# Kernel optimization log

Measured on AMD Instinct MI355X. Metric: run time of the kernel, lower is better.

## Reference

```python
import jax, jax.numpy as jnp
import numpy as np

NUM_EMB = 512
EMB_DIM = 64

def conv1d(x, w, b=None, stride=1, padding=0):
    # x: (N,C,L), w: (O,I,K) torch Conv1d layout
    out = jax.lax.conv_general_dilated(x, w, (stride,), [(padding, padding)],
                                       dimension_numbers=('NCH', 'OIH', 'NCH'))
    if b is not None:
        out = out + b[None, :, None]
    return out

def conv_transpose1d(x, w, b, stride, padding):
    # w: (I,O,K) torch ConvTranspose1d layout -> flip kernel, swap I/O
    k = w.shape[2]
    wf = jnp.flip(w, 2).transpose(1, 0, 2)  # (O,I,K)
    pad = k - 1 - padding
    out = jax.lax.conv_general_dilated(x, wf, (1,), [(pad, pad)],
                                       lhs_dilation=(stride,),
                                       dimension_numbers=('NCH', 'OIH', 'NCH'))
    return out + b[None, :, None]

def residual_block(x, w1, w2):
    # ReLU -> conv3(pad1, no bias) -> ReLU -> conv1(no bias), residual add
    h = conv1d(jax.nn.relu(x), w1, None, 1, 1)
    h = conv1d(jax.nn.relu(h), w2, None, 1, 0)
    return x + h

def residual_stack(x, r0_w1, r0_w2, r1_w1, r1_w2):
    x = residual_block(x, r0_w1, r0_w2)
    x = residual_block(x, r1_w1, r1_w2)
    return jax.nn.relu(x)

def vq(z, emb):
    # z: (B, C=64, T); torch VectorQuantizerEMA eval path (decay=0, not training)
    B, C, T = z.shape
    inputs = z.transpose(0, 2, 1)                 # (B,T,C)
    flat = inputs.reshape(-1, C)                  # (B*T, C)
    d = (jnp.sum(flat * flat, axis=1, keepdims=True)
         + jnp.sum(emb * emb, axis=1)
         - 2.0 * flat @ emb.T)                    # (B*T, K)
    idx = jnp.argmin(d, axis=1)
    enc = jax.nn.one_hot(idx, NUM_EMB, dtype=flat.dtype)  # (B*T, K)
    q = (enc @ emb).reshape(B, T, C)
    # straight-through estimator
    q = inputs + jax.lax.stop_gradient(q - inputs)
    return q.transpose(0, 2, 1)                   # (B,C,T)

def reference(x, enc_w1, enc_b1, enc_w2, enc_b2, enc_w3, enc_b3,
              enc_r0_w1, enc_r0_w2, enc_r1_w1, enc_r1_w2,
              prevq_w, prevq_b, emb,
              dec_w1, dec_b1, dec_r0_w1, dec_r0_w2, dec_r1_w1, dec_r1_w2,
              dect1_w, dect1_b, dect2_w, dect2_b):
    # Encoder
    h = jax.nn.relu(conv1d(x, enc_w1, enc_b1, 2, 1))
    h = jax.nn.relu(conv1d(h, enc_w2, enc_b2, 2, 1))
    h = conv1d(h, enc_w3, enc_b3, 1, 1)
    h = residual_stack(h, enc_r0_w1, enc_r0_w2, enc_r1_w1, enc_r1_w2)
    # pre-VQ 1x1 conv
    z = conv1d(h, prevq_w, prevq_b, 1, 0)
    # Vector quantization
    q = vq(z, emb)
    # Decoder
    d = conv1d(q, dec_w1, dec_b1, 1, 1)
    d = residual_stack(d, dec_r0_w1, dec_r0_w2, dec_r1_w1, dec_r1_w2)
    d = jax.nn.relu(conv_transpose1d(d, dect1_w, dect1_b, 2, 1))
    return conv_transpose1d(d, dect2_w, dect2_b, 2, 1)

def setup_inputs() -> dict:
    key = jax.random.key(0)
    ks = jax.random.split(key, 25)
    def n(k, shape, s=0.05):
        return jax.random.normal(k, shape, dtype=jnp.float32) * s
    return {
        'x': jax.random.normal(ks[0], (16, 768, 4096), dtype=jnp.float32),
        'enc_w1': n(ks[1], (32, 768, 4)), 'enc_b1': n(ks[2], (32,)),
        'enc_w2': n(ks[3], (64, 32, 4)), 'enc_b2': n(ks[4], (64,)),
        'enc_w3': n(ks[5], (64, 64, 3)), 'enc_b3': n(ks[6], (64,)),
        'enc_r0_w1': n(ks[7], (32, 64, 3)), 'enc_r0_w2': n(ks[8], (64, 32, 1)),
        'enc_r1_w1': n(ks[9], (32, 64, 3)), 'enc_r1_w2': n(ks[10], (64, 32, 1)),
        'prevq_w': n(ks[11], (64, 64, 1)), 'prevq_b': n(ks[12], (64,)),
        'emb': jax.random.normal(ks[13], (512, 64), dtype=jnp.float32),
        'dec_w1': n(ks[14], (64, 64, 3)), 'dec_b1': n(ks[15], (64,)),
        'dec_r0_w1': n(ks[16], (32, 64, 3)), 'dec_r0_w2': n(ks[17], (64, 32, 1)),
        'dec_r1_w1': n(ks[18], (32, 64, 3)), 'dec_r1_w2': n(ks[19], (64, 32, 1)),
        'dect1_w': n(ks[20], (64, 32, 4)), 'dect1_b': n(ks[21], (32,)),
        'dect2_w': n(ks[22], (32, 64, 4)), 'dect2_b': n(ks[23], (64,)),
    }
```

## Files before the change

### kernel.cpp

```cpp
#include <hip/hip_runtime.h>


typedef _Float16 half8 __attribute__((ext_vector_type(8)));
typedef float f32x4 __attribute__((ext_vector_type(4)));
union H8u { half8 h; int4 i; };
union P4u { _Float16 e[4]; int2 u; };

__device__ __forceinline__ void splitf(float v, _Float16& h, _Float16& l) {
  h = (_Float16)v; l = (_Float16)((v - (float)h) * 2048.0f);
}
#define INV2048 (1.0f / 2048.0f)

#define OFF_C1   0
#define OFF_C2   98304
#define OFF_C3   106496
#define OFF_ER0A 122880
#define OFF_ER0B 131072
#define OFF_ER1A 133120
#define OFF_ER1B 141312
#define OFF_PQ   143360
#define OFF_DW1  147456
#define OFF_DR0A 163840
#define OFF_DR0B 172032
#define OFF_DR1A 174080
#define OFF_DR1B 182272
#define OFF_T1   184320
#define OFF_T2   200704
#define WTOT     217088

struct WPtrs {
  const float *c1, *c2, *c3, *er0a, *er0b, *er1a, *er1b, *pq,
              *dw1, *dr0a, *dr0b, *dr1a, *dr1b, *t1, *t2;
};

__device__ __forceinline__ int tpose_kt(int par, int tap) {
  if (par == 0) { if (tap == 0) return 3; if (tap == 1) return 1; }
  else          { if (tap == 1) return 2; if (tap == 2) return 0; }
  return -1;
}

__global__ __launch_bounds__(256) void prep_k(WPtrs P, _Float16* __restrict__ WH,
                                              _Float16* __restrict__ WL) {
  int s = blockIdx.x * 256 + threadIdx.x;
  if (s >= WTOT) return;
  float v = 0.f;
  if (s < OFF_C2) {
    int t = s, kkblk = t >> 11, rem = t & 2047, col = rem >> 6, kkin = rem & 63;
    int kk = kkblk * 64 + kkin;
    v = P.c1[col * 3072 + kk];
  } else if (s < OFF_C3) {
    int t = s - OFF_C2, co = t >> 7, kk = t & 127;
    v = P.c2[(co * 32 + (kk >> 2)) * 4 + (kk & 3)];
  } else if (s < OFF_ER0A) {
    int t = s - OFF_C3, co = t >> 8, kk = t & 255, tap = kk & 3;
    if (tap < 3) v = P.c3[(co * 64 + (kk >> 2)) * 3 + tap];
  } else if (s < OFF_ER0B) {
    int t = s - OFF_ER0A, co = t >> 8, kk = t & 255, tap = kk & 3;
    if (tap < 3) v = P.er0a[(co * 64 + (kk >> 2)) * 3 + tap];
  } else if (s < OFF_ER1A) {
    int t = s - OFF_ER0B; v = P.er0b[t];
  } else if (s < OFF_ER1B) {
    int t = s - OFF_ER1A, co = t >> 8, kk = t & 255, tap = kk & 3;
    if (tap < 3) v = P.er1a[(co * 64 + (kk >> 2)) * 3 + tap];
  } else if (s < OFF_PQ) {
    int t = s - OFF_ER1B; v = P.er1b[t];
  } else if (s < OFF_DW1) {
    int t = s - OFF_PQ; v = P.pq[t];
  } else if (s < OFF_DR0A) {
    int t = s - OFF_DW1, co = t >> 8, kk = t & 255, tap = kk & 3;
    if (tap < 3) v = P.dw1[(co * 64 + (kk >> 2)) * 3 + tap];
  } else if (s < OFF_DR0B) {
    int t = s - OFF_DR0A, co = t >> 8, kk = t & 255, tap = kk & 3;
    if (tap < 3) v = P.dr0a[(co * 64 + (kk >> 2)) * 3 + tap];
  } else if (s < OFF_DR1A) {
    int t = s - OFF_DR0B; v = P.dr0b[t];
  } else if (s < OFF_DR1B) {
    int t = s - OFF_DR1A, co = t >> 8, kk = t & 255, tap = kk & 3;
    if (tap < 3) v = P.dr1a[(co * 64 + (kk >> 2)) * 3 + tap];
  } else if (s < OFF_T1) {
    int t = s - OFF_DR1B; v = P.dr1b[t];
  } else if (s < OFF_T2) {
    int t = s - OFF_T1, nn = t >> 8, kk = t & 255;
    int par = nn >> 5, co = nn & 31, ci = kk >> 2;
    int kt = tpose_kt(par, kk & 3);
    if (kt >= 0) v = P.t1[(ci * 32 + co) * 4 + kt];
  } else {
    int t = s - OFF_T2, nn = t >> 7, kk = t & 127;
    int par = nn >> 6, co = nn & 63, ci = kk >> 2;
    int kt = tpose_kt(par, kk & 3);
    if (kt >= 0) v = P.t2[(ci * 64 + co) * 4 + kt];
  }
  _Float16 h, l; splitf(v, h, l);
  WH[s] = h; WL[s] = l;
}

__global__ __launch_bounds__(256, 4) void conv1_k(
    const float* __restrict__ x, const _Float16* __restrict__ WH,
    const _Float16* __restrict__ WL, float* __restrict__ Pout, int cpp) {
  __shared__ _Float16 Hs[2][16 * 136];
  __shared__ _Float16 Ls[2][16 * 136];
  __shared__ _Float16 Bhs[2][32 * 64];
  __shared__ _Float16 Bls[2][32 * 64];
  const int tid = threadIdx.x;
  const int w = tid >> 6, lane = tid & 63, lm = lane & 15, quad = lane >> 4;
  const int m0 = blockIdx.x * 64, n = blockIdx.y, kpart = blockIdx.z;
  const int r = w * 16 + lm;
  const int pb = 2 * m0 - 1;
  const float* xn = x + (size_t)n * 768 * 4096;
  const int r0s = tid / 33, c0s = tid % 33;
  const int r1s = (256 + tid) / 33, c1s = (256 + tid) % 33;
  const int r2s = (512 + tid) / 33, c2s = (512 + tid) % 33;
  const int bcol = tid >> 3, bslot = tid & 7;
  const int bdst = bcol * 64 + ((bslot ^ (bcol & 7)) << 3);

  f32x4 acc1[2], acc2[2];
#pragma unroll
  for (int j = 0; j < 2; ++j)
#pragma unroll
    for (int rr = 0; rr < 4; ++rr) { acc1[j][rr] = 0.f; acc2[j][rr] = 0.f; }

  const int cb0 = kpart * cpp;
  float4 sv0, sv1, sv2;
  H8u bhv, blv;

#define C1_LD1(SV, RS, CS) { \
    int p0 = pb + 4 * (CS); \
    const float* rp = xn + (size_t)(chb + (RS)) * 4096; \
    if (p0 >= 0 && p0 + 3 < 4096) SV = *(const float4*)(rp + p0); \
    else { \
      SV.x = (p0   >= 0 && p0   < 4096) ? rp[p0]   : 0.f; \
      SV.y = (p0+1 >= 0 && p0+1 < 4096) ? rp[p0+1] : 0.f; \
      SV.z = (p0+2 >= 0 && p0+2 < 4096) ? rp[p0+2] : 0.f; \
      SV.w = (p0+3 >= 0 && p0+3 < 4096) ? rp[p0+3] : 0.f; } }

#define C1_LOAD(cc) { \
    int chb = (cb0 + (cc)) * 16; \
    C1_LD1(sv0, r0s, c0s) \
    C1_LD1(sv1, r1s, c1s) \
    if (tid < 16) C1_LD1(sv2, r2s, c2s) \
    bhv.i = *(const int4*)(WH + (size_t)(cb0 + (cc)) * 2048 + tid * 8); \
    blv.i = *(const int4*)(WL + (size_t)(cb0 + (cc)) * 2048 + tid * 8); }

#define C1_WR1(SV, RS, CS, B) { \
    P4u ph, pl; \
    splitf(SV.x, ph.e[0], pl.e[0]); splitf(SV.y, ph.e[1], pl.e[1]); \
    splitf(SV.z, ph.e[2], pl.e[2]); splitf(SV.w, ph.e[3], pl.e[3]); \
    *(int2*)(&Hs[B][(RS) * 136 + 4 * (CS)]) = ph.u; \
    *(int2*)(&Ls[B][(RS) * 136 + 4 * (CS)]) = pl.u; }

#define C1_WRITE(B) { \
    C1_WR1(sv0, r0s, c0s, B) \
    C1_WR1(sv1, r1s, c1s, B) \
    if (tid < 16) C1_WR1(sv2, r2s, c2s, B) \
    *(int4*)(&Bhs[B][bdst]) = bhv.i; \
    *(int4*)(&Bls[B][bdst]) = blv.i; }

#define C1_COMP(B) { \
    const uint* Hdw = (const uint*)(&Hs[B][0]); \
    const uint* Ldw = (const uint*)(&Ls[B][0]); \
    _Pragma("unroll") \
    for (int ks = 0; ks < 2; ++ks) { \
      const int ci0 = ks * 8 + quad * 2; \
      const int bse = ci0 * 68 + r; \
      H8u ah, al; \
      ah.i.x = Hdw[bse];      ah.i.y = Hdw[bse + 1]; \
      ah.i.z = Hdw[bse + 68]; ah.i.w = Hdw[bse + 69]; \
      al.i.x = Ldw[bse];      al.i.y = Ldw[bse + 1]; \
      al.i.z = Ldw[bse + 68]; al.i.w = Ldw[bse + 69]; \
      const int sA = ((4 * ks + quad) ^ (lm & 7)) << 3; \
      H8u b0h, b0l, b1h, b1l; \
      b0h.i = *(const int4*)(&Bhs[B][lm * 64 + sA]); \
      b0l.i = *(const int4*)(&Bls[B][lm * 64 + sA]); \
      b1h.i = *(const int4*)(&Bhs[B][(16 + lm) * 64 + sA]); \
      b1l.i = *(const int4*)(&Bls[B][(16 + lm) * 64 + sA]); \
      acc1[0] = __builtin_amdgcn_mfma_f32_16x16x32_f16(ah.h, b0h.h, acc1[0], 0,0,0); \
      acc2[0] = __builtin_amdgcn_mfma_f32_16x16x32_f16(ah.h, b0l.h, acc2[0], 0,0,0); \
      acc2[0] = __builtin_amdgcn_mfma_f32_16x16x32_f16(al.h, b0h.h, acc2[0], 0,0,0); \
      acc1[1] = __builtin_amdgcn_mfma_f32_16x16x32_f16(ah.h, b1h.h, acc1[1], 0,0,0); \
      acc2[1] = __builtin_amdgcn_mfma_f32_16x16x32_f16(ah.h, b1l.h, acc2[1], 0,0,0); \
      acc2[1] = __builtin_amdgcn_mfma_f32_16x16x32_f16(al.h, b1h.h, acc2[1], 0,0,0); \
    } }

  C1_LOAD(0);
  C1_WRITE(0);
  __syncthreads();
#pragma unroll 1
  for (int cc = 0; cc < cpp; ++cc) {
    const int cur = cc & 1;
    if (cc + 1 < cpp) C1_LOAD(cc + 1);
    C1_COMP(cur);
    if (cc + 1 < cpp) C1_WRITE(cur ^ 1);
    __syncthreads();
  }

#pragma unroll
  for (int j = 0; j < 2; ++j) {
    int col = j * 16 + lm;
    float4 o;
    o.x = acc1[j][0] + acc2[j][0] * INV2048;
    o.y = acc1[j][1] + acc2[j][1] * INV2048;
    o.z = acc1[j][2] + acc2[j][2] * INV2048;
    o.w = acc1[j][3] + acc2[j][3] * INV2048;
    *(float4*)(Pout + (size_t)kpart * (16 * 32 * 2048)
               + ((size_t)n * 32 + col) * 2048 + m0 + w * 16 + quad * 4) = o;
  }
#undef C1_LD1
#undef C1_LOAD
#undef C1_WR1
#undef C1_WRITE
#undef C1_COMP
}

template<int CI, int KP, int NT, int STRIDE,
         bool RELU_IN, bool RELU_OUT, bool BIAS, bool TPOSE, bool RESBLK,
         bool PSUM = false>
__global__ __launch_bounds__(256) void gconv(
    const float* __restrict__ in, const _Float16* __restrict__ WH,
    const _Float16* __restrict__ WL, const float* __restrict__ bias,
    const _Float16* __restrict__ W2H, const _Float16* __restrict__ W2L,
    float* __restrict__ out, int Lin, int Lout,
    const float* __restrict__ inbias, int nparts, int pplane) {
  constexpr int CP = 32 * STRIDE + 4;
  constexpr int CP4 = CP / 4;
  constexpr int AP = KP + 8;
  constexpr int KS = KP / 32;
  constexpr int NTW = (NT == 2) ? 1 : NT / 2;
  __shared__ float xs[CI * CP];
  __shared__ _Float16 Ah[32 * AP];
  __shared__ _Float16 Al[32 * AP];
  __shared__ _Float16 A2h[RESBLK ? 32 * 40 : 1];
  __shared__ _Float16 A2l[RESBLK ? 32 * 40 : 1];
  const int tid = threadIdx.x;
  const int w = tid >> 6, lane = tid & 63, lm = lane & 15, quad = lane >> 4;
  const int mt = w >> 1, ntb = (w & 1) * NTW;
  const int m0 = blockIdx.x * 32, n = blockIdx.y;
  const int base = m0 * STRIDE - 1;
  const float* inN = in + (size_t)n * CI * Lin;
  constexpr int SLOTS = CI * CP4;
#pragma unroll
  for (int it = 0; it < (SLOTS + 255) / 256; ++it) {
    int idx = it * 256 + tid;
    if (idx < SLOTS) {
      int row = idx / CP4, c4 = idx % CP4;
      int p0 = base + c4 * 4;
      const float* rp = inN + (size_t)row * Lin;
      float4 v;
      if (PSUM) {
        v.x = 0.f; v.y = 0.f; v.z = 0.f; v.w = 0.f;
        bool i0 = (p0   >= 0 && p0   < Lin);
        bool i1 = (p0+1 >= 0 && p0+1 < Lin);
        bool i2 = (p0+2 >= 0 && p0+2 < Lin);
        bool i3 = (p0+3 >= 0 && p0+3 < Lin);
        bool full = (p0 >= 0 && p0 + 3 < Lin);
        for (int p = 0; p < nparts; ++p) {
          const float* rpp = rp + (size_t)p * pplane;
          if (full) {
            float4 t = *(const float4*)(rpp + p0);
            v.x += t.x; v.y += t.y; v.z += t.z; v.w += t.w;
          } else {
            if (i0) v.x += rpp[p0];
            if (i1) v.y += rpp[p0+1];
            if (i2) v.z += rpp[p0+2];
            if (i3) v.w += rpp[p0+3];
          }
        }
        float bv = inbias[row];
        v.x = i0 ? fmaxf(v.x + bv, 0.f) : 0.f;
        v.y = i1 ? fmaxf(v.y + bv, 0.f) : 0.f;
        v.z = i2 ? fmaxf(v.z + bv, 0.f) : 0.f;
        v.w = i3 ? fmaxf(v.w + bv, 0.f) : 0.f;
      } else {
        if (p0 >= 0 && p0 + 3 < Lin) v = *(const float4*)(rp + p0);
        else {
          v.x = (p0   >= 0 && p0   < Lin) ? rp[p0]   : 0.f;
          v.y = (p0+1 >= 0 && p0+1 < Lin) ? rp[p0+1] : 0.f;
          v.z = (p0+2 >= 0 && p0+2 < Lin) ? rp[p0+2] : 0.f;
          v.w = (p0+3 >= 0 && p0+3 < Lin) ? rp[p0+3] : 0.f;
        }
      }
      *(float4*)(&xs[row * CP + c4 * 4]) = v;
    }
  }
  __syncthreads();
#pragma unroll
  for (int it = 0; it < (32 * CI) / 256; ++it) {
    int slot = it * 256 + tid;
    int ci = slot & (CI - 1), m = slot / CI;
    const float* xr = &xs[ci * CP + STRIDE * m];
    float a0 = xr[0], a1 = xr[1], a2 = xr[2], a3 = xr[3];
    if (RELU_IN) { a0 = fmaxf(a0,0.f); a1 = fmaxf(a1,0.f);
                   a2 = fmaxf(a2,0.f); a3 = fmaxf(a3,0.f); }
    P4u ph, pl;
    splitf(a0, ph.e[0], pl.e[0]); splitf(a1, ph.e[1], pl.e[1]);
    splitf(a2, ph.e[2], pl.e[2]); splitf(a3, ph.e[3], pl.e[3]);
    *(int2*)(&Ah[m * AP + ci * 4]) = ph.u;
    *(int2*)(&Al[m * AP + ci * 4]) = pl.u;
  }
  __syncthreads();
  f32x4 acc1[NTW], acc2[NTW];
#pragma unroll
  for (int j = 0; j < NTW; ++j)
#pragma unroll
    for (int r = 0; r < 4; ++r) { acc1[j][r] = 0.f; acc2[j][r] = 0.f; }
  H8u bh[2][NTW], bl[2][NTW];
#pragma unroll
  for (int j = 0; j < NTW; ++j) {
    int col = (ntb + j) * 16 + lm;
    bh[0][j].i = *(const int4*)(WH + (size_t)col * KP + quad * 8);
    bl[0][j].i = *(const int4*)(WL + (size_t)col * KP + quad * 8);
  }
#pragma unroll
  for (int ks = 0; ks < KS; ++ks) {
    int cur = ks & 1;
    if (ks + 1 < KS) {
#pragma unroll
      for (int j = 0; j < NTW; ++j) {
        int col = (ntb + j) * 16 + lm;
        bh[cur ^ 1][j].i = *(const int4*)(WH + (size_t)col * KP + (ks+1) * 32 + quad * 8);
        bl[cur ^ 1][j].i = *(const int4*)(WL + (size_t)col * KP + (ks+1) * 32 + quad * 8);
      }
    }
    H8u ah, al;
    ah.i = *(const int4*)(&Ah[(mt * 16 + lm) * AP + ks * 32 + quad * 8]);
    al.i = *(const int4*)(&Al[(mt * 16 + lm) * AP + ks * 32 + quad * 8]);
#pragma unroll
    for (int j = 0; j < NTW; ++j) {
      acc1[j] = __builtin_amdgcn_mfma_f32_16x16x32_f16(ah.h, bh[cur][j].h, acc1[j], 0,0,0);
      acc2[j] = __builtin_amdgcn_mfma_f32_16x16x32_f16(ah.h, bl[cur][j].h, acc2[j], 0,0,0);
      acc2[j] = __builtin_amdgcn_mfma_f32_16x16x32_f16(al.h, bh[cur][j].h, acc2[j], 0,0,0);
    }
  }
  if (RESBLK) {
    int co2 = (w & 1) * 16 + lm;
#pragma unroll
    for (int r = 0; r < 4; ++r) {
      float hv = fmaxf(acc1[0][r] + acc2[0][r] * INV2048, 0.f);
      _Float16 hh, hl; splitf(hv, hh, hl);
      int m = mt * 16 + quad * 4 + r;
      A2h[m * 40 + co2] = hh; A2l[m * 40 + co2] = hl;
    }
    __syncthreads();
    f32x4 c1[2], c2[2];
#pragma unroll
    for (int j = 0; j < 2; ++j)
#pragma unroll
      for (int r = 0; r < 4; ++r) { c1[j][r] = 0.f; c2[j][r] = 0.f; }
    H8u a2h, a2l;
    a2h.i = *(const int4*)(&A2h[(mt * 16 + lm) * 40 + quad * 8]);
    a2l.i = *(const int4*)(&A2l[(mt * 16 + lm) * 40 + quad * 8]);
    int ntb2 = (w & 1) * 2;
#pragma unroll
    for (int j = 0; j < 2; ++j) {
      int col = (ntb2 + j) * 16 + lm;
      H8u wbh, wbl;
      wbh.i = *(const int4*)(W2H + col * 32 + quad * 8);
      wbl.i = *(const int4*)(W2L + col * 32 + quad * 8);
      c1[j] = __builtin_amdgcn_mfma_f32_16x16x32_f16(a2h.h, wbh.h, c1[j], 0,0,0);
      c2[j] = __builtin_amdgcn_mfma_f32_16x16x32_f16(a2h.h, wbl.h, c2[j], 0,0,0);
      c2[j] = __builtin_amdgcn_mfma_f32_16x16x32_f16(a2l.h, wbh.h, c2[j], 0,0,0);
    }
#pragma unroll
    for (int j = 0; j < 2; ++j) {
      int col = (ntb2 + j) * 16 + lm;
      float4 o;
#pragma unroll
      for (int r = 0; r < 4; ++r) {
        int m = mt * 16 + quad * 4 + r;
        float res = xs[col * CP + m + 1];
        ((float*)&o)[r] = res + c1[j][r] + c2[j][r] * INV2048;
      }
      *(float4*)(out + ((size_t)n * 64 + col) * Lout + m0 + mt * 16 + quad * 4) = o;
    }
  } else {
    constexpr int CO = TPOSE ? NT * 8 : NT * 16;
#pragma unroll
    for (int j = 0; j < NTW; ++j) {
      int col = (ntb + j) * 16 + lm;
      int par = TPOSE ? (col / CO) : 0;
      int co  = TPOSE ? (col % CO) : col;
      float bv = BIAS ? bias[co] : 0.f;
      float vr[4];
#pragma unroll
      for (int r = 0; r < 4; ++r) {
        float v = acc1[j][r] + acc2[j][r] * INV2048 + bv;
        vr[r] = RELU_OUT ? fmaxf(v, 0.f) : v;
      }
      if (TPOSE) {
#pragma unroll
        for (int r = 0; r < 4; ++r) {
          int m = m0 + mt * 16 + quad * 4 + r;
          out[((size_t)n * CO + co) * Lout + 2 * m + par] = vr[r];
        }
      } else {
        float4 o; o.x = vr[0]; o.y = vr[1]; o.z = vr[2]; o.w = vr[3];
        *(float4*)(out + ((size_t)n * CO + co) * Lout + m0 + mt * 16 + quad * 4) = o;
      }
    }
  }
}

__global__ void enorm_k(const float* __restrict__ emb, float* __restrict__ en) {
  int e = blockIdx.x * blockDim.x + threadIdx.x;
  if (e >= 512) return;
  float s = 0.f;
  const float* r = emb + (size_t)e * 64;
  for (int c = 0; c < 64; ++c) s = fmaf(r[c], r[c], s);
  en[e] = s;
}

__global__ __launch_bounds__(256) void vq_fused(
    const float* __restrict__ sIn, const _Float16* __restrict__ PQH,
    const _Float16* __restrict__ PQL, const float* __restrict__ pqb,
    const float* __restrict__ emb, const float* __restrict__ en,
    float* __restrict__ q) {
  __shared__ float xs[64 * 68];
  __shared__ _Float16 Ah[64 * 72];
  __shared__ _Float16 Al[64 * 72];
  __shared__ float zl[64 * 65];
  __shared__ float dred[4 * 64];
  __shared__ int   ired[4 * 64];
  __shared__ int   idxs[64];
  const int tid = threadIdx.x;
  const int w = tid >> 6, lane = tid & 63, lm = lane & 15, quad = lane >> 4;
  const int n = blockIdx.y, t0 = blockIdx.x * 64;
#pragma unroll
  for (int it = 0; it < 4; ++it) {
    int idx = it * 256 + tid;
    int row = idx >> 4, c4 = idx & 15;
    float4 v = *(const float4*)(sIn + ((size_t)n * 64 + row) * 1024 + t0 + c4 * 4);
    *(float4*)(&xs[row * 68 + c4 * 4]) = v;
  }
  __syncthreads();
#pragma unroll
  for (int it = 0; it < 16; ++it) {
    int slot = it * 256 + tid;
    int ci = slot & 63, t = slot >> 6;
    float v = fmaxf(xs[ci * 68 + t], 0.f);
    _Float16 h, l; splitf(v, h, l);
    Ah[t * 72 + ci] = h; Al[t * 72 + ci] = l;
  }
  __syncthreads();
  f32x4 a1[4], a2[4];
#pragma unroll
  for (int j = 0; j < 4; ++j)
#pragma unroll
    for (int r = 0; r < 4; ++r) { a1[j][r] = 0.f; a2[j][r] = 0.f; }
#pragma unroll
  for (int ks = 0; ks < 2; ++ks) {
    H8u ah, al;
    ah.i = *(const int4*)(&Ah[(w * 16 + lm) * 72 + ks * 32 + quad * 8]);
    al.i = *(const int4*)(&Al[(w * 16 + lm) * 72 + ks * 32 + quad * 8]);
#pragma unroll
    for (int j = 0; j < 4; ++j) {
      int col = j * 16 + lm;
      H8u bh, bl;
      bh.i = *(const int4*)(PQH + col * 64 + ks * 32 + quad * 8);
      bl.i = *(const int4*)(PQL + col * 64 + ks * 32 + quad * 8);
      a1[j] = __builtin_amdgcn_mfma_f32_16x16x32_f16(ah.h, bh.h, a1[j], 0,0,0);
      a2[j] = __builtin_amdgcn_mfma_f32_16x16x32_f16(ah.h, bl.h, a2[j], 0,0,0);
      a2[j] = __builtin_amdgcn_mfma_f32_16x16x32_f16(al.h, bh.h, a2[j], 0,0,0);
    }
  }
#pragma unroll
  for (int j = 0; j < 4; ++j) {
    int col = j * 16 + lm;
    float bv = pqb[col];
#pragma unroll
    for (int r = 0; r < 4; ++r) {
      int t = w * 16 + quad * 4 + r;
      zl[t * 65 + col] = a1[j][r] + a2[j][r] * INV2048 + bv;
    }
  }
  __syncthreads();
  int tt = tid & 63, cq = tid >> 6;
  float zv[64];
#pragma unroll
  for (int c = 0; c < 64; ++c) zv[c] = zl[tt * 65 + c];
  float best = 1e30f; int bidx = 0;
  for (int e = cq * 128; e < cq * 128 + 128; ++e) {
    const float* er = emb + (size_t)e * 64;
    float dot = 0.f;
#pragma unroll
    for (int c = 0; c < 64; ++c) dot = fmaf(zv[c], er[c], dot);
    float d = en[e] - 2.f * dot;
    if (d < best) { best = d; bidx = e; }
  }
  dred[cq * 64 + tt] = best;
  ired[cq * 64 + tt] = bidx;
  __syncthreads();
  if (cq == 0) {
    for (int j = 1; j < 4; ++j) {
      float d = dred[j * 64 + tt]; int i2 = ired[j * 64 + tt];
      if (d < best || (d == best && i2 < bidx)) { best = d; bidx = i2; }
    }
    idxs[tt] = bidx;
  }
  __syncthreads();
  for (int it = 0; it < 16; ++it) {
    int c = cq * 16 + it;
    q[((size_t)n * 64 + c) * 1024 + t0 + tt] = emb[(size_t)idxs[tt] * 64 + c];
  }
}

extern "C" void kernel_launch(void* const* d_in, const int* in_sizes, int n_in,
                              void* d_out, int out_size, void* d_ws, size_t ws_size,
                              hipStream_t stream) {
  const float* x        = (const float*)d_in[0];
  const float* enc_b1   = (const float*)d_in[2];
  const float* enc_b2   = (const float*)d_in[4];
  const float* enc_b3   = (const float*)d_in[6];
  const float* prevq_b  = (const float*)d_in[12];
  const float* emb      = (const float*)d_in[13];
  const float* dec_b1   = (const float*)d_in[15];
  const float* dect1_b  = (const float*)d_in[21];
  const float* dect2_b  = (const float*)d_in[23];
  float* out = (float*)d_out;

  WPtrs P;
  P.c1  = (const float*)d_in[1];  P.c2  = (const float*)d_in[3];
  P.c3  = (const float*)d_in[5];  P.er0a = (const float*)d_in[7];
  P.er0b = (const float*)d_in[8]; P.er1a = (const float*)d_in[9];
  P.er1b = (const float*)d_in[10]; P.pq = (const float*)d_in[11];
  P.dw1 = (const float*)d_in[14]; P.dr0a = (const float*)d_in[16];
  P.dr0b = (const float*)d_in[17]; P.dr1a = (const float*)d_in[18];
  P.dr1b = (const float*)d_in[19]; P.t1 = (const float*)d_in[20];
  P.t2  = (const float*)d_in[22];

  float* A  = (float*)d_ws;
  float* B  = A + (1u << 20);
  float* EN = B + (1u << 20);
  _Float16* WH = (_Float16*)(EN + 1024);
  _Float16* WL = WH + WTOT;
  float* PP = (float*)(WL + WTOT);

  const size_t baseBytes = (size_t)((char*)PP - (char*)d_ws);
  const size_t planeB = (size_t)16 * 32 * 2048 * 4;
  int nparts = 1;
  float* Pbuf = A;
  if (ws_size >= baseBytes + 2 * planeB) { nparts = 2; Pbuf = PP; }

  dim3 blk(256);
  prep_k<<<dim3((WTOT + 255) / 256), blk, 0, stream>>>(P, WH, WL);
  enorm_k<<<dim3(2), blk, 0, stream>>>(emb, EN);
  conv1_k<<<dim3(32, 16, nparts), blk, 0, stream>>>(x, WH + OFF_C1, WL + OFF_C1,
                                                    Pbuf, 48 / nparts);
  gconv<32,128,4,2, false,true,true, false,false, true><<<dim3(32,16), blk, 0, stream>>>(
      Pbuf, WH+OFF_C2, WL+OFF_C2, enc_b2, nullptr, nullptr, B, 2048, 1024,
      enc_b1, nparts, 16 * 32 * 2048);
  gconv<64,256,4,1, false,false,true, false,false><<<dim3(32,16), blk, 0, stream>>>(
      B, WH+OFF_C3, WL+OFF_C3, enc_b3, nullptr, nullptr, A, 1024, 1024,
      nullptr, 1, 0);
  gconv<64,256,2,1, true,false,false, false,true><<<dim3(32,16), blk, 0, stream>>>(
      A, WH+OFF_ER0A, WL+OFF_ER0A, nullptr, WH+OFF_ER0B, WL+OFF_ER0B, B, 1024, 1024,
      nullptr, 1, 0);
  gconv<64,256,2,1, true,false,false, false,true><<<dim3(32,16), blk, 0, stream>>>(
      B, WH+OFF_ER1A, WL+OFF_ER1A, nullptr, WH+OFF_ER1B, WL+OFF_ER1B, A, 1024, 1024,
      nullptr, 1, 0);
  vq_fused<<<dim3(16,16), blk, 0, stream>>>(A, WH+OFF_PQ, WL+OFF_PQ, prevq_b, emb, EN, B);
  gconv<64,256,4,1, false,false,true, false,false><<<dim3(32,16), blk, 0, stream>>>(
      B, WH+OFF_DW1, WL+OFF_DW1, dec_b1, nullptr, nullptr, A, 1024, 1024,
      nullptr, 1, 0);
  gconv<64,256,2,1, true,false,false, false,true><<<dim3(32,16), blk, 0, stream>>>(
      A, WH+OFF_DR0A, WL+OFF_DR0A, nullptr, WH+OFF_DR0B, WL+OFF_DR0B, B, 1024, 1024,
      nullptr, 1, 0);
  gconv<64,256,2,1, true,false,false, false,true><<<dim3(32,16), blk, 0, stream>>>(
      B, WH+OFF_DR1A, WL+OFF_DR1A, nullptr, WH+OFF_DR1B, WL+OFF_DR1B, A, 1024, 1024,
      nullptr, 1, 0);
  gconv<64,256,4,1, true,true,true, true,false><<<dim3(32,16), blk, 0, stream>>>(
      A, WH+OFF_T1, WL+OFF_T1, dect1_b, nullptr, nullptr, B, 1024, 2048,
      nullptr, 1, 0);
  gconv<32,128,8,1, false,false,true, true,false><<<dim3(64,16), blk, 0, stream>>>(
      B, WH+OFF_T2, WL+OFF_T2, dect2_b, nullptr, nullptr, out, 2048, 4096,
      nullptr, 1, 0);
}
```

Before: 549.5 us.

## Fuse conv3 and two residual blocks into one halo-tiled kernel

Result: no change. 544.5 us (-0.9%).

```diff
diff --git a/kernel.cpp b/kernel.cpp
--- a/kernel.cpp
+++ b/kernel.cpp
@@ -211,6 +211,243 @@
 #undef C1_COMP
 }
 
+template<int NTW_>
+__device__ __forceinline__ void k3_mfma(
+    const _Float16* __restrict__ AGH, const _Float16* __restrict__ AGL,
+    int arow, const _Float16* __restrict__ WHp, const _Float16* __restrict__ WLp,
+    int colb, int lm, int quad, f32x4 (&a1)[NTW_], f32x4 (&a2)[NTW_]) {
+  H8u bh[2][NTW_], bl[2][NTW_];
+#pragma unroll
+  for (int j = 0; j < NTW_; ++j) {
+    int col = colb + j * 16 + lm;
+    bh[0][j].i = *(const int4*)(WHp + (size_t)col * 256 + quad * 8);
+    bl[0][j].i = *(const int4*)(WLp + (size_t)col * 256 + quad * 8);
+  }
+#pragma unroll
+  for (int ks = 0; ks < 8; ++ks) {
+    int cur = ks & 1;
+    if (ks + 1 < 8) {
+#pragma unroll
+      for (int j = 0; j < NTW_; ++j) {
+        int col = colb + j * 16 + lm;
+        bh[cur ^ 1][j].i = *(const int4*)(WHp + (size_t)col * 256 + (ks+1) * 32 + quad * 8);
+        bl[cur ^ 1][j].i = *(const int4*)(WLp + (size_t)col * 256 + (ks+1) * 32 + quad * 8);
+      }
+    }
+    H8u ah, al;
+    ah.i = *(const int4*)(&AGH[(arow + lm) * 264 + ks * 32 + quad * 8]);
+    al.i = *(const int4*)(&AGL[(arow + lm) * 264 + ks * 32 + quad * 8]);
+#pragma unroll
+    for (int j = 0; j < NTW_; ++j) {
+      a1[j] = __builtin_amdgcn_mfma_f32_16x16x32_f16(ah.h, bh[cur][j].h, a1[j], 0,0,0);
+      a2[j] = __builtin_amdgcn_mfma_f32_16x16x32_f16(ah.h, bl[cur][j].h, a2[j], 0,0,0);
+      a2[j] = __builtin_amdgcn_mfma_f32_16x16x32_f16(al.h, bh[cur][j].h, a2[j], 0,0,0);
+    }
+  }
+}
+
+__global__ __launch_bounds__(256, 2) void stack3_k(
+    const float* __restrict__ in,
+    const _Float16* __restrict__ WAH, const _Float16* __restrict__ WAL,
+    const float* __restrict__ biasA,
+    const _Float16* __restrict__ W0AH, const _Float16* __restrict__ W0AL,
+    const _Float16* __restrict__ W0BH, const _Float16* __restrict__ W0BL,
+    const _Float16* __restrict__ W1AH, const _Float16* __restrict__ W1AL,
+    const _Float16* __restrict__ W1BH, const _Float16* __restrict__ W1BL,
+    float* __restrict__ out) {
+  __shared__ float XS[64 * 68];
+  __shared__ float HP[64 * 68];
+  __shared__ float RP[32 * 52];
+  __shared__ _Float16 AGH[32 * 264];
+  __shared__ _Float16 AGL[32 * 264];
+  const int tid = threadIdx.x;
+  const int w = tid >> 6, lane = tid & 63, lm = lane & 15, quad = lane >> 4;
+  const int m0 = blockIdx.x * 32, n = blockIdx.y;
+  const float* inN = in + (size_t)n * 64 * 1024;
+
+  {
+    const int pb = m0 - 17;
+#pragma unroll
+    for (int it = 0; it < 5; ++it) {
+      int idx = it * 256 + tid;
+      if (idx < 64 * 17) {
+        int row = idx / 17, c4 = idx % 17;
+        int p0 = pb + c4 * 4;
+        const float* rp = inN + (size_t)row * 1024;
+        float4 v;
+        if (p0 >= 0 && p0 + 3 < 1024) v = *(const float4*)(rp + p0);
+        else {
+          v.x = (p0   >= 0 && p0   < 1024) ? rp[p0]   : 0.f;
+          v.y = (p0+1 >= 0 && p0+1 < 1024) ? rp[p0+1] : 0.f;
+          v.z = (p0+2 >= 0 && p0+2 < 1024) ? rp[p0+2] : 0.f;
+          v.w = (p0+3 >= 0 && p0+3 < 1024) ? rp[p0+3] : 0.f;
+        }
+        *(float4*)(&XS[row * 68 + c4 * 4]) = v;
+      }
+    }
+  }
+  __syncthreads();
+
+#define GATH64(SRC, SSTR, OFS, ROWS, RELUF) { \
+    _Pragma("unroll") \
+    for (int it = 0; it < (ROWS) / 4; ++it) { \
+      int slot = it * 256 + tid; \
+      int ci = slot & 63, m = slot >> 6; \
+      const float* xr = &SRC[ci * (SSTR) + (OFS) + m]; \
+      float a0 = xr[0], a1v = xr[1], a2v = xr[2], a3 = xr[3]; \
+      if (RELUF) { a0 = fmaxf(a0,0.f); a1v = fmaxf(a1v,0.f); \
+                   a2v = fmaxf(a2v,0.f); a3 = fmaxf(a3,0.f); } \
+      P4u ph, pl; \
+      splitf(a0, ph.e[0], pl.e[0]); splitf(a1v, ph.e[1], pl.e[1]); \
+      splitf(a2v, ph.e[2], pl.e[2]); splitf(a3, ph.e[3], pl.e[3]); \
+      *(int2*)(&AGH[m * 264 + ci * 4]) = ph.u; \
+      *(int2*)(&AGL[m * 264 + ci * 4]) = pl.u; } }
+
+#pragma unroll
+  for (int P = 0; P < 2; ++P) {
+    GATH64(XS, 68, P * 32, 32, false);
+    __syncthreads();
+    {
+      f32x4 a1[2], a2[2];
+#pragma unroll
+      for (int j = 0; j < 2; ++j)
+#pragma unroll
+        for (int rr = 0; rr < 4; ++rr) { a1[j][rr] = 0.f; a2[j][rr] = 0.f; }
+      k3_mfma<2>(AGH, AGL, (w >> 1) * 16, WAH, WAL, (w & 1) * 32, lm, quad, a1, a2);
+#pragma unroll
+      for (int j = 0; j < 2; ++j) {
+        int col = (w & 1) * 32 + j * 16 + lm;
+        float bv = biasA[col];
+#pragma unroll
+        for (int rr = 0; rr < 4; ++rr) {
+          int m = (w >> 1) * 16 + quad * 4 + rr;
+          int qh = P * 32 + m;
+          int gp = m0 - 16 + qh;
+          float hv = a1[j][rr] + a2[j][rr] * INV2048 + bv;
+          HP[col * 68 + qh] = (gp >= 0 && gp < 1024) ? hv : 0.f;
+        }
+      }
+    }
+    __syncthreads();
+  }
+
+  GATH64(HP, 68, 7, 32, true);
+  __syncthreads();
+  {
+    f32x4 a1[1], a2[1];
+#pragma unroll
+    for (int rr = 0; rr < 4; ++rr) { a1[0][rr] = 0.f; a2[0][rr] = 0.f; }
+    k3_mfma<1>(AGH, AGL, (w >> 1) * 16, W0AH, W0AL, (w & 1) * 16, lm, quad, a1, a2);
+    int col2 = (w & 1) * 16 + lm;
+#pragma unroll
+    for (int rr = 0; rr < 4; ++rr) {
+      int m = (w >> 1) * 16 + quad * 4 + rr;
+      RP[col2 * 52 + m] = a1[0][rr] + a2[0][rr] * INV2048;
+    }
+  }
+  __syncthreads();
+  GATH64(HP, 68, 39, 16, true);
+  __syncthreads();
+  if ((w >> 1) == 0) {
+    f32x4 a1[1], a2[1];
+#pragma unroll
+    for (int rr = 0; rr < 4; ++rr) { a1[0][rr] = 0.f; a2[0][rr] = 0.f; }
+    k3_mfma<1>(AGH, AGL, 0, W0AH, W0AL, (w & 1) * 16, lm, quad, a1, a2);
+    int col2 = (w & 1) * 16 + lm;
+#pragma unroll
+    for (int rr = 0; rr < 4; ++rr) {
+      int m = quad * 4 + rr;
+      RP[col2 * 52 + 32 + m] = a1[0][rr] + a2[0][rr] * INV2048;
+    }
+  }
+  __syncthreads();
+
+#pragma unroll
+  for (int it = 0; it < 6; ++it) {
+    int slot = it * 256 + tid;
+    int ci = slot & 31, m = slot >> 5;
+    float v = fmaxf(RP[ci * 52 + m], 0.f);
+    _Float16 h, l; splitf(v, h, l);
+    AGH[m * 40 + ci] = h; AGL[m * 40 + ci] = l;
+  }
+  __syncthreads();
+  {
+    int col = w * 16 + lm;
+    H8u wbh, wbl;
+    wbh.i = *(const int4*)(W0BH + col * 32 + quad * 8);
+    wbl.i = *(const int4*)(W0BL + col * 32 + quad * 8);
+#pragma unroll
+    for (int mt2 = 0; mt2 < 3; ++mt2) {
+      f32x4 c1 = {0.f,0.f,0.f,0.f}, c2 = {0.f,0.f,0.f,0.f};
+      H8u a2h, a2l;
+      a2h.i = *(const int4*)(&AGH[(mt2 * 16 + lm) * 40 + quad * 8]);
+      a2l.i = *(const int4*)(&AGL[(mt2 * 16 + lm) * 40 + quad * 8]);
+      c1 = __builtin_amdgcn_mfma_f32_16x16x32_f16(a2h.h, wbh.h, c1, 0,0,0);
+      c2 = __builtin_amdgcn_mfma_f32_16x16x32_f16(a2h.h, wbl.h, c2, 0,0,0);
+      c2 = __builtin_amdgcn_mfma_f32_16x16x32_f16(a2l.h, wbh.h, c2, 0,0,0);
+#pragma unroll
+      for (int rr = 0; rr < 4; ++rr) {
+        int qs = mt2 * 16 + quad * 4 + rr;
+        int gp = m0 - 8 + qs;
+        float sv = HP[col * 68 + qs + 8] + c1[rr] + c2[rr] * INV2048;
+        XS[col * 52 + qs] = (gp >= 0 && gp < 1024) ? sv : 0.f;
+      }
+    }
+  }
+  __syncthreads();
+
+  GATH64(XS, 52, 7, 32, true);
+  __syncthreads();
+  {
+    f32x4 a1[1], a2[1];
+#pragma unroll
+    for (int rr = 0; rr < 4; ++rr) { a1[0][rr] = 0.f; a2[0][rr] = 0.f; }
+    k3_mfma<1>(AGH, AGL, (w >> 1) * 16, W1AH, W1AL, (w & 1) * 16, lm, quad, a1, a2);
+    int col2 = (w & 1) * 16 + lm;
+#pragma unroll
+    for (int rr = 0; rr < 4; ++rr) {
+      int m = (w >> 1) * 16 + quad * 4 + rr;
+      RP[col2 * 52 + m] = a1[0][rr] + a2[0][rr] * INV2048;
+    }
+  }
+  __syncthreads();
+
+#pragma unroll
+  for (int it = 0; it < 4; ++it) {
+    int slot = it * 256 + tid;
+    int ci = slot & 31, m = slot >> 5;
+    float v = fmaxf(RP[ci * 52 + m], 0.f);
+    _Float16 h, l; splitf(v, h, l);
+    AGH[m * 40 + ci] = h; AGL[m * 40 + ci] = l;
+  }
+  __syncthreads();
+  {
+    int mt2 = w >> 1, ntb2 = (w & 1) * 2;
+    H8u a2h, a2l;
+    a2h.i = *(const int4*)(&AGH[(mt2 * 16 + lm) * 40 + quad * 8]);
+    a2l.i = *(const int4*)(&AGL[(mt2 * 16 + lm) * 40 + quad * 8]);
+#pragma unroll
+    for (int j = 0; j < 2; ++j) {
+      int col = (ntb2 + j) * 16 + lm;
+      H8u wbh, wbl;
+      wbh.i = *(const int4*)(W1BH + col * 32 + quad * 8);
+      wbl.i = *(const int4*)(W1BL + col * 32 + quad * 8);
+      f32x4 c1 = {0.f,0.f,0.f,0.f}, c2 = {0.f,0.f,0.f,0.f};
+      c1 = __builtin_amdgcn_mfma_f32_16x16x32_f16(a2h.h, wbh.h, c1, 0,0,0);
+      c2 = __builtin_amdgcn_mfma_f32_16x16x32_f16(a2h.h, wbl.h, c2, 0,0,0);
+      c2 = __builtin_amdgcn_mfma_f32_16x16x32_f16(a2l.h, wbh.h, c2, 0,0,0);
+      float4 o;
+#pragma unroll
+      for (int rr = 0; rr < 4; ++rr) {
+        int m = mt2 * 16 + quad * 4 + rr;
+        ((float*)&o)[rr] = XS[col * 52 + m + 8] + c1[rr] + c2[rr] * INV2048;
+      }
+      *(float4*)(out + ((size_t)n * 64 + col) * 1024 + m0 + mt2 * 16 + quad * 4) = o;
+    }
+  }
+#undef GATH64
+}
+
 template<int CI, int KP, int NT, int STRIDE,
          bool RELU_IN, bool RELU_OUT, bool BIAS, bool TPOSE, bool RESBLK,
          bool PSUM = false>
@@ -547,25 +784,15 @@
   gconv<32,128,4,2, false,true,true, false,false, true><<<dim3(32,16), blk, 0, stream>>>(
       Pbuf, WH+OFF_C2, WL+OFF_C2, enc_b2, nullptr, nullptr, B, 2048, 1024,
       enc_b1, nparts, 16 * 32 * 2048);
-  gconv<64,256,4,1, false,false,true, false,false><<<dim3(32,16), blk, 0, stream>>>(
-      B, WH+OFF_C3, WL+OFF_C3, enc_b3, nullptr, nullptr, A, 1024, 1024,
-      nullptr, 1, 0);
-  gconv<64,256,2,1, true,false,false, false,true><<<dim3(32,16), blk, 0, stream>>>(
-      A, WH+OFF_ER0A, WL+OFF_ER0A, nullptr, WH+OFF_ER0B, WL+OFF_ER0B, B, 1024, 1024,
-      nullptr, 1, 0);
-  gconv<64,256,2,1, true,false,false, false,true><<<dim3(32,16), blk, 0, stream>>>(
-      B, WH+OFF_ER1A, WL+OFF_ER1A, nullptr, WH+OFF_ER1B, WL+OFF_ER1B, A, 1024, 1024,
-      nullptr, 1, 0);
+  stack3_k<<<dim3(32,16), blk, 0, stream>>>(
+      B, WH+OFF_C3, WL+OFF_C3, enc_b3,
+      WH+OFF_ER0A, WL+OFF_ER0A, WH+OFF_ER0B, WL+OFF_ER0B,
+      WH+OFF_ER1A, WL+OFF_ER1A, WH+OFF_ER1B, WL+OFF_ER1B, A);
   vq_fused<<<dim3(16,16), blk, 0, stream>>>(A, WH+OFF_PQ, WL+OFF_PQ, prevq_b, emb, EN, B);
-  gconv<64,256,4,1, false,false,true, false,false><<<dim3(32,16), blk, 0, stream>>>(
-      B, WH+OFF_DW1, WL+OFF_DW1, dec_b1, nullptr, nullptr, A, 1024, 1024,
-      nullptr, 1, 0);
-  gconv<64,256,2,1, true,false,false, false,true><<<dim3(32,16), blk, 0, stream>>>(
-      A, WH+OFF_DR0A, WL+OFF_DR0A, nullptr, WH+OFF_DR0B, WL+OFF_DR0B, B, 1024, 1024,
-      nullptr, 1, 0);
-  gconv<64,256,2,1, true,false,false, false,true><<<dim3(32,16), blk, 0, stream>>>(
-      B, WH+OFF_DR1A, WL+OFF_DR1A, nullptr, WH+OFF_DR1B, WL+OFF_DR1B, A, 1024, 1024,
-      nullptr, 1, 0);
+  stack3_k<<<dim3(32,16), blk, 0, stream>>>(
+      B, WH+OFF_DW1, WL+OFF_DW1, dec_b1,
+      WH+OFF_DR0A, WL+OFF_DR0A, WH+OFF_DR0B, WL+OFF_DR0B,
+      WH+OFF_DR1A, WL+OFF_DR1A, WH+OFF_DR1B, WL+OFF_DR1B, A);
   gconv<64,256,4,1, true,true,true, true,false><<<dim3(32,16), blk, 0, stream>>>(
       A, WH+OFF_T1, WL+OFF_T1, dect1_b, nullptr, nullptr, B, 1024, 2048,
       nullptr, 1, 0);
```
